# Performance work log

Hardware: AMD Instinct MI355X
Metric: run time of the kernel (lower is better)

## Reference

```python
import jax, jax.numpy as jnp
import numpy as np

EPS = 1e-5

def _bn(y, gamma, beta):
    # BatchNorm1d in training mode over the flattened (B*N, C) batch dim.
    m = jnp.mean(y, axis=0)
    v = jnp.var(y, axis=0)  # biased variance, matches torch normalization
    return gamma * (y - m) * jax.lax.rsqrt(v + EPS) + beta

def _hardswish(x):
    return x * jnp.clip(x + 3.0, 0.0, 6.0) / 6.0

def setup_inputs() -> dict:
    key = jax.random.key(0)
    ks = jax.random.split(key, 8)
    B, N, C, H = 16, 784, 384, 8
    res = int(N ** 0.5)  # 28
    inner = 3 * C
    x = jax.random.normal(ks[0], (B, N, C), dtype=jnp.float32)
    Wqkv = jax.random.normal(ks[1], (inner, C), dtype=jnp.float32) * (C ** -0.5)
    g1 = jnp.ones((inner,), jnp.float32) + 0.1 * jax.random.normal(ks[2], (inner,))
    b1 = 0.1 * jax.random.normal(ks[3], (inner,))
    Wproj = jax.random.normal(ks[4], (C, C), dtype=jnp.float32) * (C ** -0.5)
    g2 = jnp.ones((C,), jnp.float32) + 0.1 * jax.random.normal(ks[5], (C,))
    b2 = 0.1 * jax.random.normal(ks[6], (C,))
    biases = 0.02 * jax.random.normal(ks[7], (H, res * res), dtype=jnp.float32)
    # idx[i,j] = |dx|*res + |dy| reproduces torch's encounter-order offset ids
    coords = np.stack(np.meshgrid(np.arange(res), np.arange(res), indexing='ij'), -1).reshape(N, 2)
    d = np.abs(coords[:, None, :] - coords[None, :, :])
    bias_idxs = jnp.asarray(d[..., 0] * res + d[..., 1], dtype=jnp.int32)  # [N,N]
    return {"x": x, "Wqkv": Wqkv, "g1": g1, "b1": b1, "Wproj": Wproj,
            "g2": g2, "b2": b2, "biases": biases, "bias_idxs": bias_idxs}

def reference(x, Wqkv, g1, b1, Wproj, g2, b2, biases, bias_idxs):
    B, N, C = x.shape
    H = biases.shape[0]
    hd = C // H
    scale = hd ** -0.5
    # qkv = LinearNorm(dim, 3*dim)
    y = _bn(x.reshape(B * N, C) @ Wqkv.T, g1, b1)              # [B*N, 3C]
    qkv = y.reshape(B, N, 3, H, hd).transpose(2, 0, 3, 1, 4)   # [3,B,H,N,hd]
    q, k, v = qkv[0], qkv[1], qkv[2]
    attn = jnp.einsum('bhnd,bhmd->bhnm', q, k) * scale         # [B,H,N,N]
    attn = attn + biases[:, bias_idxs][None]                   # gathered rel-pos bias
    attn = jax.nn.softmax(attn, axis=-1)
    o = jnp.einsum('bhnm,bhmd->bhnd', attn, v)                 # [B,H,N,hd]
    o = o.transpose(0, 2, 1, 3).reshape(B, N, C)
    # proj = Hardswish -> LinearNorm(dim, dim)
    o = _hardswish(o).reshape(B * N, C)
    o = _bn(o @ Wproj.T, g2, b2)
    return o.reshape(B, N, C)
```

## Files before the change

### kernel.cpp

```cpp
#include <hip/hip_runtime.h>

#define R_TOTAL 12544
#define NTOK    784
#define CDIM    384
#define INNER   1152
#define NHEAD   8
#define HDIM    48
#define BATCH   16
#define HSEG    37632
#define SCALE   0.14433756729740643f
#define LOG2E   1.4426950408889634f
#define SCLOG2E 0.20823509f

typedef unsigned short u16;
typedef unsigned int   u32;
typedef __attribute__((ext_vector_type(8))) short short8;
typedef __attribute__((ext_vector_type(4))) float floatx4;

union V8 { uint4 u; short8 s; u16 h[8]; };

#define OB_OFF     28901376ull
#define ST_OFF     38535168ull

__device__ __forceinline__ float b2f(u16 u) {
    union { float f; u32 i; } v; v.i = ((u32)u) << 16; return v.f;
}
__device__ __forceinline__ u16 f2b(float f) {
    union { float f; u32 i; } v; v.f = f;
    u32 r = v.i + 0x7FFFu + ((v.i >> 16) & 1u);
    return (u16)(r >> 16);
}
__device__ __forceinline__ u32 pk2(float lo, float hi) {
    union { float f; u32 i; } a, b; a.f = lo; b.f = hi;
    u32 ra = a.i + 0x7FFFu + ((a.i >> 16) & 1u);
    u32 rb = b.i + 0x7FFFu + ((b.i >> 16) & 1u);
    return __builtin_amdgcn_perm(rb, ra, 0x07060302u);
}
__device__ __forceinline__ float hswish_f(float v) {
    return v * fminf(fmaxf(v + 3.f, 0.f), 6.f) * (1.f / 6.f);
}

__device__ __forceinline__ void gll16(const void* g, void* l) {
    __builtin_amdgcn_global_load_lds(
        (const __attribute__((address_space(1))) void*)g,
        (__attribute__((address_space(3))) void*)l, 16, 0, 0);
}

__global__ __launch_bounds__(256) void zero_k(float* __restrict__ p, int n) {
    int i = blockIdx.x * 256 + threadIdx.x;
    if (i < n) p[i] = 0.f;
}

__global__ __launch_bounds__(256) void cvt8_k(
    const float* __restrict__ src, u16* __restrict__ dst, int total8)
{
    int i = blockIdx.x * 256 + threadIdx.x;
    if (i >= total8) return;
    const float* p = src + (size_t)i * 8;
    float4 f0 = *(const float4*)p, f1 = *(const float4*)(p + 4);
    uint4 o;
    o.x = pk2(f0.x, f0.y); o.y = pk2(f0.z, f0.w);
    o.z = pk2(f1.x, f1.y); o.w = pk2(f1.z, f1.w);
    *(uint4*)(dst + (size_t)i * 8) = o;
}

template<int OBF16, int HEADM>
__global__ __launch_bounds__(256) void gemm_bb_k(
    const u16* __restrict__ A, const u16* __restrict__ B,
    void* __restrict__ Cp, float* __restrict__ sums, int Nout, int K)
{
    __shared__ u16 As[128 * 32];
    __shared__ u16 Bs[128 * 32];
    const int t = threadIdx.x;
    const int lane = t & 63, wv = t >> 6;
    const int l15 = lane & 15, quad = lane >> 4;
    const int wm = (wv & 1) * 64, wn = (wv >> 1) * 64;
    const int m0 = blockIdx.y * 128, n0 = blockIdx.x * 128;
    const floatx4 zf = {0.f, 0.f, 0.f, 0.f};

    floatx4 acc[4][4];
    #pragma unroll
    for (int i = 0; i < 4; i++)
        #pragma unroll
        for (int j = 0; j < 4; j++) acc[i][j] = zf;

    for (int k0 = 0; k0 < K; k0 += 32) {
        __syncthreads();
        #pragma unroll
        for (int it = 0; it < 2; it++) {
            const int flat = t + it * 256;
            const int rr = flat >> 2, ss = (flat & 3) * 8;
            gll16(A + (size_t)(m0 + rr) * K + k0 + ss, As + (size_t)flat * 8);
            gll16(B + (size_t)(n0 + rr) * K + k0 + ss, Bs + (size_t)flat * 8);
        }
        asm volatile("s_waitcnt vmcnt(0)" ::: "memory");
        __syncthreads();
        short8 af[4], bfr[4];
        #pragma unroll
        for (int mi = 0; mi < 4; mi++)
            af[mi] = *(const short8*)&As[(wm + mi * 16 + l15) * 32 + quad * 8];
        #pragma unroll
        for (int ni = 0; ni < 4; ni++)
            bfr[ni] = *(const short8*)&Bs[(wn + ni * 16 + l15) * 32 + quad * 8];
        #pragma unroll
        for (int mi = 0; mi < 4; mi++)
            #pragma unroll
            for (int ni = 0; ni < 4; ni++)
                acc[mi][ni] = __builtin_amdgcn_mfma_f32_16x16x32_bf16(af[mi], bfr[ni], acc[mi][ni], 0, 0, 0);
    }

    float cs[4] = {0.f, 0.f, 0.f, 0.f}, cq[4] = {0.f, 0.f, 0.f, 0.f};
    #pragma unroll
    for (int mi = 0; mi < 4; mi++) {
        const int mbase = m0 + wm + mi * 16 + quad * 4;
        int bb_[4], nn_[4];
        if (HEADM) {
            #pragma unroll
            for (int reg = 0; reg < 4; reg++) {
                int m = mbase + reg;
                int bv = ((m >> 4) * 1338) >> 16;
                bb_[reg] = bv;
                nn_[reg] = m - bv * 784;
            }
        }
        #pragma unroll
        for (int ni = 0; ni < 4; ni++) {
            const int c0 = n0 + wn + ni * 16;
            const int n = c0 + l15;
            int part = 0, hcol = 0, d0 = 0;
            if (HEADM) {
                part = c0 / 384;
                int rem = c0 - part * 384;
                hcol = rem / 48;
                d0 = rem - hcol * 48;
            }
            if (HEADM && part == 2) {
                u32 w0 = pk2(acc[mi][ni][0], acc[mi][ni][1]);
                u32 w1 = pk2(acc[mi][ni][2], acc[mi][ni][3]);
                size_t off = (size_t)((bb_[0] * 8 + hcol) * 3 + 2) * HSEG
                           + (size_t)(d0 + l15) * NTOK + nn_[0];
                *(uint2*)((u16*)Cp + off) = make_uint2(w0, w1);
                float v0 = b2f((u16)(w0 & 0xffff)), v1 = b2f((u16)(w0 >> 16));
                float v2 = b2f((u16)(w1 & 0xffff)), v3 = b2f((u16)(w1 >> 16));
                cs[ni] += (v0 + v1) + (v2 + v3);
                cq[ni] += (v0 * v0 + v1 * v1) + (v2 * v2 + v3 * v3);
            } else {
                #pragma unroll
                for (int reg = 0; reg < 4; reg++) {
                    float v = acc[mi][ni][reg];
                    float vv;
                    if (OBF16) {
                        u16 hv = f2b(v);
                        size_t off;
                        if (HEADM)
                            off = (size_t)((bb_[reg] * 8 + hcol) * 3 + part) * HSEG
                                + (size_t)nn_[reg] * 48 + d0 + l15;
                        else
                            off = (size_t)(mbase + reg) * Nout + n;
                        ((u16*)Cp)[off] = hv;
                        vv = b2f(hv);
                    } else {
                        ((float*)Cp)[(size_t)(mbase + reg) * Nout + n] = v;
                        vv = v;
                    }
                    cs[ni] += vv;
                    cq[ni] += vv * vv;
                }
            }
        }
    }
    #pragma unroll
    for (int ni = 0; ni < 4; ni++) {
        float s = cs[ni], sq = cq[ni];
        s  += __shfl_xor(s, 16);  s  += __shfl_xor(s, 32);
        sq += __shfl_xor(sq, 16); sq += __shfl_xor(sq, 32);
        if (quad == 0) {
            int col = n0 + wn + ni * 16 + l15;
            atomicAdd(&sums[col], s);
            atomicAdd(&sums[Nout + col], sq);
        }
    }
}

__global__ __launch_bounds__(256) void finalize_bn_k(
    const float* __restrict__ sums, const float* __restrict__ g,
    const float* __restrict__ bvec, float* __restrict__ ab, int Ncols, float invM,
    int sc0, int sc1, float sfac)
{
    int c = blockIdx.x * 256 + threadIdx.x;
    if (c >= Ncols) return;
    float mean = sums[c] * invM;
    float var  = sums[Ncols + c] * invM - mean * mean;
    float a    = g[c] * rsqrtf(var + 1e-5f);
    float f    = (c >= sc0 && c < sc1) ? sfac : 1.f;
    ab[c] = a * f;
    ab[Ncols + c] = (bvec[c] - mean * a) * f;
}

__global__ __launch_bounds__(256) void bn_apply_k(
    float* __restrict__ Z, const float* __restrict__ ab, int Ncols, int total4)
{
    for (int i4 = blockIdx.x * 256 + threadIdx.x; i4 < total4; i4 += gridDim.x * 256) {
        int col = (i4 * 4) % Ncols;
        float4 z  = *(float4*)(Z + (size_t)i4 * 4);
        float4 a4 = *(const float4*)(ab + col);
        float4 b4 = *(const float4*)(ab + Ncols + col);
        z.x = a4.x * z.x + b4.x; z.y = a4.y * z.y + b4.y;
        z.z = a4.z * z.z + b4.z; z.w = a4.w * z.w + b4.w;
        *(float4*)(Z + (size_t)i4 * 4) = z;
    }
}

__global__ __launch_bounds__(256) void bn_apply_bf16_k(
    u16* __restrict__ Z, const float* __restrict__ ab, int total8)
{
    int i8 = blockIdx.x * 256 + threadIdx.x;
    if (i8 >= total8) return;
    int e0  = i8 * 8;
    int seg = e0 / HSEG;
    int rem = e0 - seg * HSEG;
    int part = seg % 3;
    int hh   = (seg / 3) & 7;
    uint4 u = *(uint4*)(Z + (size_t)i8 * 8);
    uint4 o;
    if (part == 2) {
        int dd  = rem / NTOK;
        int col = 2 * 384 + hh * 48 + dd;
        float a = ab[col], bb = ab[1152 + col];
        o.x = pk2(fmaf(b2f((u16)(u.x & 0xffff)), a, bb), fmaf(b2f((u16)(u.x >> 16)), a, bb));
        o.y = pk2(fmaf(b2f((u16)(u.y & 0xffff)), a, bb), fmaf(b2f((u16)(u.y >> 16)), a, bb));
        o.z = pk2(fmaf(b2f((u16)(u.z & 0xffff)), a, bb), fmaf(b2f((u16)(u.z >> 16)), a, bb));
        o.w = pk2(fmaf(b2f((u16)(u.w & 0xffff)), a, bb), fmaf(b2f((u16)(u.w >> 16)), a, bb));
    } else {
        int d0  = rem % 48;
        int col = part * 384 + hh * 48 + d0;
        float4 A0 = *(const float4*)(ab + col),        A1 = *(const float4*)(ab + col + 4);
        float4 B0 = *(const float4*)(ab + 1152 + col), B1 = *(const float4*)(ab + 1152 + col + 4);
        o.x = pk2(fmaf(b2f((u16)(u.x & 0xffff)), A0.x, B0.x), fmaf(b2f((u16)(u.x >> 16)), A0.y, B0.y));
        o.y = pk2(fmaf(b2f((u16)(u.y & 0xffff)), A0.z, B0.z), fmaf(b2f((u16)(u.y >> 16)), A0.w, B0.w));
        o.z = pk2(fmaf(b2f((u16)(u.z & 0xffff)), A1.x, B1.x), fmaf(b2f((u16)(u.z >> 16)), A1.y, B1.y));
        o.w = pk2(fmaf(b2f((u16)(u.w & 0xffff)), A1.z, B1.z), fmaf(b2f((u16)(u.w >> 16)), A1.w, B1.w));
    }
    *(uint4*)(Z + (size_t)i8 * 8) = o;
}

__global__ __launch_bounds__(256) void attn_mfma_k(
    const u16* __restrict__ Y,
    const float* __restrict__ biases, const int* __restrict__ idxs,
    u16* __restrict__ O)
{
    __shared__ u16 psm[4][2][2 * 64 * 8];
    __shared__ float hb[NTOK];

    const int t = threadIdx.x;
    const int lane = t & 63, wv = t >> 6;
    const int l15 = lane & 15, quad = lane >> 4;
    const int bh = blockIdx.x;
    const int b = bh >> 3, h = bh & 7;
    const int n0 = blockIdx.y * 128;
    const int bN = b * NTOK;
    const floatx4 zf = {0.f, 0.f, 0.f, 0.f};

    const u16* Qb = Y + (size_t)(bh * 3) * HSEG;
    const u16* Kb = Qb + HSEG;
    const u16* Vb = Qb + 2 * HSEG;

    if (t < 196) {
        float4 v = *(const float4*)(biases + (size_t)h * NTOK + (t << 2));
        v.x *= LOG2E; v.y *= LOG2E; v.z *= LOG2E; v.w *= LOG2E;
        *(float4*)&hb[t << 2] = v;
    }

    int qv[2], qr[2];
    #pragma unroll
    for (int qh = 0; qh < 2; qh++) {
        qv[qh] = n0 + qh * 64 + wv * 16 + l15;
        qr[qh] = qv[qh] < NTOK ? qv[qh] : NTOK - 1;
    }
    const int* idxrow[2] = { idxs + (size_t)qr[0] * NTOK, idxs + (size_t)qr[1] * NTOK };

    short8 qf[2][2];
    #pragma unroll
    for (int qh = 0; qh < 2; qh++) {
        V8 a0, a1;
        a1.u = make_uint4(0u, 0u, 0u, 0u);
        const u16* src = Qb + (size_t)qr[qh] * 48;
        a0.u = *(const uint4*)(src + quad * 8);
        if (quad < 2) a1.u = *(const uint4*)(src + 32 + quad * 8);
        qf[qh][0] = a0.s; qf[qh][1] = a1.s;
    }

    V8 kfr[4][2];
    #pragma unroll
    for (int sub = 0; sub < 4; sub++) {
        const u16* src = Kb + (size_t)(sub * 16 + l15) * 48;
        kfr[sub][0].u = *(const uint4*)(src + quad * 8);
        kfr[sub][1].u = *(const uint4*)(src + 32 + quad * 8);
    }

    float lsum[2] = {0.f, 0.f};
    floatx4 oacc[2][3];
    #pragma unroll
    for (int qh = 0; qh < 2; qh++)
        #pragma unroll
        for (int i = 0; i < 3; i++) oacc[qh][i] = zf;

    const int psbase = ((quad >> 1) * 16 + l15) * 8 + (quad & 1) * 4;

    __syncthreads();

    for (int mt = 0; mt < 13; mt++) {
        const int m0k = mt * 64;
        const bool tail = (m0k == 768);

        int4 ivc[2][4];
        #pragma unroll
        for (int qh = 0; qh < 2; qh++)
            #pragma unroll
            for (int sub = 0; sub < 4; sub++) {
                int kb = m0k + sub * 16 + quad * 4;
                kb = kb < NTOK - 4 ? kb : NTOK - 4;
                ivc[qh][sub] = *(const int4*)(idxrow[qh] + kb);
            }

        short8 vfr[2][3];
        #pragma unroll
        for (int kc = 0; kc < 2; kc++) {
            int kk = m0k + kc * 32 + quad * 8;
            kk = kk <= NTOK - 8 ? kk : 0;
            #pragma unroll
            for (int ns = 0; ns < 3; ns++)
                vfr[kc][ns] = *(const short8*)(Vb + (size_t)(ns * 16 + l15) * NTOK + kk);
        }

        V8 kn[4][2];
        const bool more = (mt + 1 < 13);
        if (more) {
            const int mn = m0k + 64;
            #pragma unroll
            for (int sub = 0; sub < 4; sub++) {
                int key = mn + sub * 16 + l15;
                int kr  = key < NTOK ? key : NTOK - 1;
                const u16* src = Kb + (size_t)kr * 48;
                kn[sub][0].u = *(const uint4*)(src + quad * 8);
                kn[sub][1].u = *(const uint4*)(src + 32 + quad * 8);
            }
        }

        #pragma unroll
        for (int qh = 0; qh < 2; qh++) {
            floatx4 sf[4];
            #pragma unroll
            for (int sub = 0; sub < 4; sub++) {
                floatx4 c = zf;
                c = __builtin_amdgcn_mfma_f32_16x16x32_bf16(kfr[sub][0].s, qf[qh][0], c, 0, 0, 0);
                c = __builtin_amdgcn_mfma_f32_16x16x32_bf16(kfr[sub][1].s, qf[qh][1], c, 0, 0, 0);
                sf[sub] = c;
            }
            #pragma unroll
            for (int sub = 0; sub < 4; sub++) {
                const int4 iv = ivc[qh][sub];
                float a0 = sf[sub][0] + hb[iv.x];
                float a1 = sf[sub][1] + hb[iv.y];
                float a2 = sf[sub][2] + hb[iv.z];
                float a3 = sf[sub][3] + hb[iv.w];
                float pr[4];
                asm("v_exp_f32 %0, %1" : "=v"(pr[0]) : "v"(a0));
                asm("v_exp_f32 %0, %1" : "=v"(pr[1]) : "v"(a1));
                asm("v_exp_f32 %0, %1" : "=v"(pr[2]) : "v"(a2));
                asm("v_exp_f32 %0, %1" : "=v"(pr[3]) : "v"(a3));
                if (tail) {
                    const int kb0 = m0k + sub * 16 + quad * 4;
                    #pragma unroll
                    for (int reg = 0; reg < 4; reg++)
                        if (kb0 + reg >= NTOK) pr[reg] = 0.f;
                }
                lsum[qh] += (pr[0] + pr[1]) + (pr[2] + pr[3]);
                int addr = psbase + (sub >> 1) * 512 + (sub & 1) * 256;
                *(uint2*)&psm[wv][qh][addr] = make_uint2(pk2(pr[0], pr[1]), pk2(pr[2], pr[3]));
            }
        }

        #pragma unroll
        for (int kc = 0; kc < 2; kc++) {
            short8 pb0 = *(const short8*)&psm[wv][0][(kc * 64 + lane) * 8];
            short8 pb1 = *(const short8*)&psm[wv][1][(kc * 64 + lane) * 8];
            #pragma unroll
            for (int ns = 0; ns < 3; ns++) {
                oacc[0][ns] = __builtin_amdgcn_mfma_f32_16x16x32_bf16(vfr[kc][ns], pb0, oacc[0][ns], 0, 0, 0);
                oacc[1][ns] = __builtin_amdgcn_mfma_f32_16x16x32_bf16(vfr[kc][ns], pb1, oacc[1][ns], 0, 0, 0);
            }
        }

        if (more) {
            #pragma unroll
            for (int sub = 0; sub < 4; sub++) {
                kfr[sub][0] = kn[sub][0];
                kfr[sub][1] = kn[sub][1];
            }
        }
    }

    #pragma unroll
    for (int qh = 0; qh < 2; qh++) {
        float ls = lsum[qh];
        ls += __shfl_xor(ls, 16);
        ls += __shfl_xor(ls, 32);
        if (qv[qh] < NTOK) {
            float rl = 1.f / ls;
            u16* dst = O + (size_t)(bN + qv[qh]) * CDIM + h * HDIM;
            #pragma unroll
            for (int ns = 0; ns < 3; ns++)
                #pragma unroll
                for (int reg = 0; reg < 4; reg++)
                    dst[ns * 16 + quad * 4 + reg] = f2b(hswish_f(oacc[qh][ns][reg] * rl));
        }
    }
}

extern "C" void kernel_launch(void* const* d_in, const int* in_sizes, int n_in,
                              void* d_out, int out_size, void* d_ws, size_t ws_size,
                              hipStream_t stream)
{
    const float* x     = (const float*)d_in[0];
    const float* Wqkv  = (const float*)d_in[1];
    const float* g1    = (const float*)d_in[2];
    const float* b1    = (const float*)d_in[3];
    const float* Wproj = (const float*)d_in[4];
    const float* g2    = (const float*)d_in[5];
    const float* b2    = (const float*)d_in[6];
    const float* bias  = (const float*)d_in[7];
    const int*   idxs  = (const int*)d_in[8];
    float* out = (float*)d_out;
    char*  wsb = (char*)d_ws;

    u16*   Yb  = (u16*)wsb;
    u16*   Ob  = (u16*)(wsb + OB_OFF);
    float* S1  = (float*)(wsb + ST_OFF);
    float* AB1 = S1 + 2304;
    float* S2  = AB1 + 2304;
    float* AB2 = S2 + 768;

    u16* xb  = (u16*)(wsb + OB_OFF);
    u16* wqb = (u16*)d_out;
    u16* wpb = (u16*)wsb;

    cvt8_k<<<(R_TOTAL * CDIM / 8 + 255) / 256, 256, 0, stream>>>(x, xb, R_TOTAL * CDIM / 8);
    cvt8_k<<<(INNER * CDIM / 8 + 255) / 256, 256, 0, stream>>>(Wqkv, wqb, INNER * CDIM / 8);
    zero_k<<<24, 256, 0, stream>>>(S1, 6144);

    gemm_bb_k<1, 1><<<dim3(INNER / 128, R_TOTAL / 128), 256, 0, stream>>>(
        xb, wqb, Yb, S1, INNER, CDIM);

    finalize_bn_k<<<(INNER + 255) / 256, 256, 0, stream>>>(
        S1, g1, b1, AB1, INNER, 1.f / R_TOTAL, CDIM, 2 * CDIM, SCLOG2E);
    bn_apply_bf16_k<<<(R_TOTAL * INNER / 8 + 255) / 256, 256, 0, stream>>>(
        Yb, AB1, R_TOTAL * INNER / 8);

    attn_mfma_k<<<dim3(NHEAD * BATCH, 7), 256, 0, stream>>>(Yb, bias, idxs, Ob);

    cvt8_k<<<(CDIM * CDIM / 8 + 255) / 256, 256, 0, stream>>>(Wproj, wpb, CDIM * CDIM / 8);
    gemm_bb_k<0, 0><<<dim3(CDIM / 128, R_TOTAL / 128), 256, 0, stream>>>(
        Ob, wpb, out, S2, CDIM, CDIM);

    finalize_bn_k<<<(CDIM + 255) / 256, 256, 0, stream>>>(
        S2, g2, b2, AB2, CDIM, 1.f / R_TOTAL, 0, 0, 1.f);
    bn_apply_k<<<1024, 256, 0, stream>>>(out, AB2, CDIM, (R_TOTAL * CDIM) / 4);
}
```

Baseline: 241.0 us.

## Precompute exp of relative-position bias table and feed P directly into MFMA

Adds a kernel that builds a per-head fp16 table of exp(bias[idx]) over the full N×N grid, so the attention kernel multiplies exp(score) by the table value instead of gathering through the index array and LDS bias row. The attention kernel also drops the LDS round-trip for the probability tile: it packs P into registers and uses the 16x16x16 bf16 MFMA with per-sub V fragments laid out to match. This removes LDS traffic and the dependent index gathers, but adds an extra pass writing about 10 MB of fp16 table, stored temporarily in the output buffer. It also doubles the MFMA instruction count at half the K depth, and rounding exp(bias) to fp16 changes precision slightly.

```diff
diff --git a/kernel.cpp b/kernel.cpp
--- a/kernel.cpp
+++ b/kernel.cpp
@@ -11,16 +11,21 @@
 #define SCALE   0.14433756729740643f
 #define LOG2E   1.4426950408889634f
 #define SCLOG2E 0.20823509f
+#define NTOK2   (NTOK * NTOK)
 
 typedef unsigned short u16;
 typedef unsigned int   u32;
 typedef __attribute__((ext_vector_type(8))) short short8;
+typedef __attribute__((ext_vector_type(4))) short s4v;
 typedef __attribute__((ext_vector_type(4))) float floatx4;
 
-union V8 { uint4 u; short8 s; u16 h[8]; };
+union V8  { uint4 u; short8 s; u16 h[8]; };
+union U2S { uint2 u; s4v s; };
+union V4H { uint2 u; _Float16 h[4]; };
 
 #define OB_OFF     28901376ull
 #define ST_OFF     38535168ull
+#define WQB_BOFF   10485760ull
 
 __device__ __forceinline__ float b2f(u16 u) {
     union { float f; u32 i; } v; v.i = ((u32)u) << 16; return v.f;
@@ -44,6 +49,15 @@
     __builtin_amdgcn_global_load_lds(
         (const __attribute__((address_space(1))) void*)g,
         (__attribute__((address_space(3))) void*)l, 16, 0, 0);
+}
+
+__device__ __forceinline__ floatx4 mfma16(s4v a, s4v b, floatx4 c) {
+#if __has_builtin(__builtin_amdgcn_mfma_f32_16x16x16bf16_1k)
+    return __builtin_amdgcn_mfma_f32_16x16x16bf16_1k(a, b, c, 0, 0, 0);
+#else
+    asm("v_mfma_f32_16x16x16_bf16 %0, %1, %2, %0" : "+v"(c) : "v"(a), "v"(b));
+    return c;
+#endif
 }
 
 __global__ __launch_bounds__(256) void zero_k(float* __restrict__ p, int n) {
@@ -62,6 +76,26 @@
     o.x = pk2(f0.x, f0.y); o.y = pk2(f0.z, f0.w);
     o.z = pk2(f1.x, f1.y); o.w = pk2(f1.z, f1.w);
     *(uint4*)(dst + (size_t)i * 8) = o;
+}
+
+__global__ __launch_bounds__(256) void eb_k(
+    const float* __restrict__ biases, const int* __restrict__ idxs,
+    u16* __restrict__ EB)
+{
+    __shared__ float eb[NTOK];
+    const int h = blockIdx.y;
+    for (int i = threadIdx.x; i < NTOK; i += 256)
+        eb[i] = exp2f(biases[(size_t)h * NTOK + i] * LOG2E);
+    __syncthreads();
+    int i4 = blockIdx.x * 256 + threadIdx.x;
+    if (i4 >= NTOK2 / 4) return;
+    int4 iv = *(const int4*)(idxs + (size_t)i4 * 4);
+    V4H o;
+    o.h[0] = (_Float16)eb[iv.x];
+    o.h[1] = (_Float16)eb[iv.y];
+    o.h[2] = (_Float16)eb[iv.z];
+    o.h[3] = (_Float16)eb[iv.w];
+    *(uint2*)(EB + (size_t)h * NTOK2 + (size_t)i4 * 4) = o.u;
 }
 
 template<int OBF16, int HEADM>
@@ -245,13 +279,9 @@
 }
 
 __global__ __launch_bounds__(256) void attn_mfma_k(
-    const u16* __restrict__ Y,
-    const float* __restrict__ biases, const int* __restrict__ idxs,
+    const u16* __restrict__ Y, const u16* __restrict__ EB,
     u16* __restrict__ O)
 {
-    __shared__ u16 psm[4][2][2 * 64 * 8];
-    __shared__ float hb[NTOK];
-
     const int t = threadIdx.x;
     const int lane = t & 63, wv = t >> 6;
     const int l15 = lane & 15, quad = lane >> 4;
@@ -264,12 +294,7 @@
     const u16* Qb = Y + (size_t)(bh * 3) * HSEG;
     const u16* Kb = Qb + HSEG;
     const u16* Vb = Qb + 2 * HSEG;
-
-    if (t < 196) {
-        float4 v = *(const float4*)(biases + (size_t)h * NTOK + (t << 2));
-        v.x *= LOG2E; v.y *= LOG2E; v.z *= LOG2E; v.w *= LOG2E;
-        *(float4*)&hb[t << 2] = v;
-    }
+    const u16* EBh = EB + (size_t)h * NTOK2;
 
     int qv[2], qr[2];
     #pragma unroll
@@ -277,7 +302,7 @@
         qv[qh] = n0 + qh * 64 + wv * 16 + l15;
         qr[qh] = qv[qh] < NTOK ? qv[qh] : NTOK - 1;
     }
-    const int* idxrow[2] = { idxs + (size_t)qr[0] * NTOK, idxs + (size_t)qr[1] * NTOK };
+    const u16* ebrow[2] = { EBh + (size_t)qr[0] * NTOK, EBh + (size_t)qr[1] * NTOK };
 
     short8 qf[2][2];
     #pragma unroll
@@ -305,32 +330,28 @@
         #pragma unroll
         for (int i = 0; i < 3; i++) oacc[qh][i] = zf;
 
-    const int psbase = ((quad >> 1) * 16 + l15) * 8 + (quad & 1) * 4;
-
-    __syncthreads();
-
     for (int mt = 0; mt < 13; mt++) {
         const int m0k = mt * 64;
         const bool tail = (m0k == 768);
 
-        int4 ivc[2][4];
+        uint2 ev[2][4];
         #pragma unroll
         for (int qh = 0; qh < 2; qh++)
             #pragma unroll
             for (int sub = 0; sub < 4; sub++) {
                 int kb = m0k + sub * 16 + quad * 4;
                 kb = kb < NTOK - 4 ? kb : NTOK - 4;
-                ivc[qh][sub] = *(const int4*)(idxrow[qh] + kb);
-            }
-
-        short8 vfr[2][3];
-        #pragma unroll
-        for (int kc = 0; kc < 2; kc++) {
-            int kk = m0k + kc * 32 + quad * 8;
-            kk = kk <= NTOK - 8 ? kk : 0;
+                ev[qh][sub] = *(const uint2*)(ebrow[qh] + kb);
+            }
+
+        U2S va[4][3];
+        #pragma unroll
+        for (int sub = 0; sub < 4; sub++) {
+            int kk = m0k + sub * 16 + quad * 4;
+            kk = kk < NTOK - 4 ? kk : NTOK - 4;
             #pragma unroll
             for (int ns = 0; ns < 3; ns++)
-                vfr[kc][ns] = *(const short8*)(Vb + (size_t)(ns * 16 + l15) * NTOK + kk);
+                va[sub][ns].u = *(const uint2*)(Vb + (size_t)(ns * 16 + l15) * NTOK + kk);
         }
 
         V8 kn[4][2];
@@ -359,16 +380,16 @@
             }
             #pragma unroll
             for (int sub = 0; sub < 4; sub++) {
-                const int4 iv = ivc[qh][sub];
-                float a0 = sf[sub][0] + hb[iv.x];
-                float a1 = sf[sub][1] + hb[iv.y];
-                float a2 = sf[sub][2] + hb[iv.z];
-                float a3 = sf[sub][3] + hb[iv.w];
-                float pr[4];
-                asm("v_exp_f32 %0, %1" : "=v"(pr[0]) : "v"(a0));
-                asm("v_exp_f32 %0, %1" : "=v"(pr[1]) : "v"(a1));
-                asm("v_exp_f32 %0, %1" : "=v"(pr[2]) : "v"(a2));
-                asm("v_exp_f32 %0, %1" : "=v"(pr[3]) : "v"(a3));
+                V4H e; e.u = ev[qh][sub];
+                float ex[4], pr[4];
+                asm("v_exp_f32 %0, %1" : "=v"(ex[0]) : "v"(sf[sub][0]));
+                asm("v_exp_f32 %0, %1" : "=v"(ex[1]) : "v"(sf[sub][1]));
+                asm("v_exp_f32 %0, %1" : "=v"(ex[2]) : "v"(sf[sub][2]));
+                asm("v_exp_f32 %0, %1" : "=v"(ex[3]) : "v"(sf[sub][3]));
+                pr[0] = ex[0] * (float)e.h[0];
+                pr[1] = ex[1] * (float)e.h[1];
+                pr[2] = ex[2] * (float)e.h[2];
+                pr[3] = ex[3] * (float)e.h[3];
                 if (tail) {
                     const int kb0 = m0k + sub * 16 + quad * 4;
                     #pragma unroll
@@ -376,19 +397,11 @@
                         if (kb0 + reg >= NTOK) pr[reg] = 0.f;
                 }
                 lsum[qh] += (pr[0] + pr[1]) + (pr[2] + pr[3]);
-                int addr = psbase + (sub >> 1) * 512 + (sub & 1) * 256;
-                *(uint2*)&psm[wv][qh][addr] = make_uint2(pk2(pr[0], pr[1]), pk2(pr[2], pr[3]));
-            }
-        }
-
-        #pragma unroll
-        for (int kc = 0; kc < 2; kc++) {
-            short8 pb0 = *(const short8*)&psm[wv][0][(kc * 64 + lane) * 8];
-            short8 pb1 = *(const short8*)&psm[wv][1][(kc * 64 + lane) * 8];
-            #pragma unroll
-            for (int ns = 0; ns < 3; ns++) {
-                oacc[0][ns] = __builtin_amdgcn_mfma_f32_16x16x32_bf16(vfr[kc][ns], pb0, oacc[0][ns], 0, 0, 0);
-                oacc[1][ns] = __builtin_amdgcn_mfma_f32_16x16x32_bf16(vfr[kc][ns], pb1, oacc[1][ns], 0, 0, 0);
+                U2S pb;
+                pb.u = make_uint2(pk2(pr[0], pr[1]), pk2(pr[2], pr[3]));
+                #pragma unroll
+                for (int ns = 0; ns < 3; ns++)
+                    oacc[qh][ns] = mfma16(va[sub][ns].s, pb.s, oacc[qh][ns]);
             }
         }
 
@@ -441,12 +454,14 @@
     float* S2  = AB1 + 2304;
     float* AB2 = S2 + 768;
 
+    u16* EB  = (u16*)d_out;
+    u16* wqb = (u16*)((char*)d_out + WQB_BOFF);
     u16* xb  = (u16*)(wsb + OB_OFF);
-    u16* wqb = (u16*)d_out;
     u16* wpb = (u16*)wsb;
 
     cvt8_k<<<(R_TOTAL * CDIM / 8 + 255) / 256, 256, 0, stream>>>(x, xb, R_TOTAL * CDIM / 8);
     cvt8_k<<<(INNER * CDIM / 8 + 255) / 256, 256, 0, stream>>>(Wqkv, wqb, INNER * CDIM / 8);
+    eb_k<<<dim3((NTOK2 / 4 + 255) / 256, NHEAD), 256, 0, stream>>>(bias, idxs, EB);
     zero_k<<<24, 256, 0, stream>>>(S1, 6144);
 
     gemm_bb_k<1, 1><<<dim3(INNER / 128, R_TOTAL / 128), 256, 0, stream>>>(
@@ -457,7 +472,7 @@
     bn_apply_bf16_k<<<(R_TOTAL * INNER / 8 + 255) / 256, 256, 0, stream>>>(
         Yb, AB1, R_TOTAL * INNER / 8);
 
-    attn_mfma_k<<<dim3(NHEAD * BATCH, 7), 256, 0, stream>>>(Yb, bias, idxs, Ob);
+    attn_mfma_k<<<dim3(NHEAD * BATCH, 7), 256, 0, stream>>>(Yb, EB, Ob);
 
     cvt8_k<<<(CDIM * CDIM / 8 + 255) / 256, 256, 0, stream>>>(Wproj, wpb, CDIM * CDIM / 8);
     gemm_bb_k<0, 0><<<dim3(CDIM / 128, R_TOTAL / 128), 256, 0, stream>>>(
```

Measured after the change: 257.3 us. 6.8% more time.
